# Performance work log

Measured on AMD Instinct MI355X. Metric: run time of the kernel, lower is better.

## Reference

```python
import jax, jax.numpy as jnp
import numpy as np

B, S, HID = 1, 2048, 2048
N_HEADS = 16
HEAD_DIM = HID // N_HEADS  # 128
ROPE_THETA = 10000.0
NEG_INF = -1e9


def setup_inputs() -> dict:
    key = jax.random.key(0)
    ks = jax.random.split(key, 5)
    hidden_states = jax.random.normal(ks[0], (B, S, HID), dtype=jnp.float32)
    scale = 1.0 / np.sqrt(HID)
    Wq = jax.random.normal(ks[1], (HID, HID), dtype=jnp.float32) * scale
    Wk = jax.random.normal(ks[2], (HID, HID), dtype=jnp.float32) * scale
    Wv = jax.random.normal(ks[3], (HID, HID), dtype=jnp.float32) * scale
    Wo = jax.random.normal(ks[4], (HID, HID), dtype=jnp.float32) * scale
    # additive causal mask [B, 1, S, S]: 0 on/below diag, -1e9 above
    causal = jnp.tril(jnp.ones((S, S), dtype=bool))
    attention_mask = jnp.where(causal, 0.0, NEG_INF).astype(jnp.float32)[None, None]
    attention_mask = jnp.broadcast_to(attention_mask, (B, 1, S, S))
    position_ids = jnp.broadcast_to(jnp.arange(S, dtype=jnp.int64)[None, :], (B, S))
    return {"hidden_states": hidden_states, "Wq": Wq, "Wk": Wk, "Wv": Wv,
            "Wo": Wo, "attention_mask": attention_mask, "position_ids": position_ids}


def _rotate_half(x):
    x1, x2 = jnp.split(x, 2, axis=-1)
    return jnp.concatenate((-x2, x1), axis=-1)


def _rope_cos_sin(position_ids, head_dim, dtype):
    inv_freq = 1.0 / (ROPE_THETA ** (jnp.arange(0, head_dim, 2, dtype=jnp.float32) / head_dim))
    freqs = position_ids.astype(jnp.float32)[:, :, None] * inv_freq[None, None, :]  # [b, s, d/2]
    emb = jnp.concatenate((freqs, freqs), axis=-1)  # [b, s, d]
    # unsqueeze_dim=1 -> broadcast over heads
    return jnp.cos(emb).astype(dtype)[:, None], jnp.sin(emb).astype(dtype)[:, None]


def reference(hidden_states, Wq, Wk, Wv, Wo, attention_mask, position_ids):
    b, s, h = hidden_states.shape
    d = HEAD_DIM
    def proj(W):
        return (hidden_states @ W.T).reshape(b, s, N_HEADS, d).transpose(0, 2, 1, 3)  # [b,h,s,d]
    q, k, v = proj(Wq), proj(Wk), proj(Wv)
    cos, sin = _rope_cos_sin(position_ids, d, q.dtype)
    q = q * cos + _rotate_half(q) * sin
    k = k * cos + _rotate_half(k) * sin
    scores = jnp.einsum('bhqd,bhkd->bhqk', q, k) / jnp.sqrt(jnp.float32(d))
    scores = scores + attention_mask
    probs = jax.nn.softmax(scores.astype(jnp.float32), axis=-1).astype(q.dtype)
    attn = jnp.einsum('bhqk,bhkd->bhqd', probs, v)
    out = attn.transpose(0, 2, 1, 3).reshape(b, s, h)
    return out @ Wo.T
```

## Files before the change

kernel.cpp:

```cpp
#include <hip/hip_runtime.h>

typedef _Float16 half8 __attribute__((ext_vector_type(8)));
typedef _Float16 half4 __attribute__((ext_vector_type(4)));
typedef float floatx4 __attribute__((ext_vector_type(4)));
typedef float floatx16 __attribute__((ext_vector_type(16)));

#define GLDS(gp, lp) __builtin_amdgcn_global_load_lds( \
    (const __attribute__((address_space(1))) void*)(gp), \
    (__attribute__((address_space(3))) void*)(lp), 16, 0, 0)

__global__ void cvt_f2h5(const float* __restrict__ s0, const float* __restrict__ s1,
                         const float* __restrict__ s2, const float* __restrict__ s3,
                         const float* __restrict__ s4,
                         _Float16* __restrict__ d0, _Float16* __restrict__ d1,
                         _Float16* __restrict__ d2, _Float16* __restrict__ d3,
                         _Float16* __restrict__ d4, int n8) {
  int i = blockIdx.x * 256 + threadIdx.x;
  if (i >= n8) return;
  const float* s; _Float16* d;
  switch (blockIdx.y) {
    case 0: s = s0; d = d0; break;
    case 1: s = s1; d = d1; break;
    case 2: s = s2; d = d2; break;
    case 3: s = s3; d = d3; break;
    default: s = s4; d = d4; break;
  }
  const float4* s4p = (const float4*)s;
  float4 a = s4p[2 * i], b = s4p[2 * i + 1];
  half8 h;
  h[0] = (_Float16)a.x; h[1] = (_Float16)a.y; h[2] = (_Float16)a.z; h[3] = (_Float16)a.w;
  h[4] = (_Float16)b.x; h[5] = (_Float16)b.y; h[6] = (_Float16)b.z; h[7] = (_Float16)b.w;
  *(half8*)(d + 8 * (size_t)i) = h;
}

__global__ __launch_bounds__(256) void transpose_k(const _Float16* __restrict__ src,
                                                   _Float16* __restrict__ dst) {
  __shared__ _Float16 t[64][72];
  const int r0 = blockIdx.y * 64, c0 = blockIdx.x * 64;
  const int tr = threadIdx.x >> 3, tc = (threadIdx.x & 7) * 8;
  #pragma unroll
  for (int p = 0; p < 2; ++p) {
    half8 v = *(const half8*)(src + (size_t)(r0 + p * 32 + tr) * 2048 + c0 + tc);
    *(half8*)&t[p * 32 + tr][tc] = v;
  }
  __syncthreads();
  #pragma unroll
  for (int p = 0; p < 2; ++p) {
    half8 v;
    #pragma unroll
    for (int j = 0; j < 8; ++j) v[j] = t[tc + j][p * 32 + tr];
    *(half8*)(dst + (size_t)(c0 + p * 32 + tr) * 2048 + r0 + tc) = v;
  }
}

__global__ __launch_bounds__(512, 1) void gemm_qkv(const _Float16* __restrict__ A,
                                                   const _Float16* __restrict__ W,
                                                   _Float16* __restrict__ Cq) {
  extern __shared__ _Float16 lds[];
  _Float16* As = lds;
  _Float16* Bs = lds + 3 * 16384;

  const int tid = threadIdx.x, lane = tid & 63, wv = tid >> 6;
  const int fr = lane & 15, fg = lane >> 4;
  const int wm = wv >> 2, wn = wv & 3;
  const int bm = blockIdx.y * 256, bn = blockIdx.x * 192;
  const _Float16* Ab = A + (size_t)bm * 2048;
  const _Float16* Bb = W + (size_t)bn * 2048;

  const int srow = lane >> 3;
  const int sgr = (lane & 7) ^ srow;

  auto stageA = [&](int t) {
    _Float16* dst = As + (t % 3) * 16384;
    const size_t coff = (size_t)t * 64 + sgr * 8;
    #pragma unroll
    for (int i = 0; i < 4; ++i) {
      const int rb = wv * 32 + i * 8;
      GLDS(Ab + (size_t)(rb + srow) * 2048 + coff, dst + rb * 64);
    }
  };
  auto stageB = [&](int t) {
    _Float16* dst = Bs + (t & 1) * 12288;
    const size_t coff = (size_t)t * 64 + sgr * 8;
    #pragma unroll
    for (int i = 0; i < 3; ++i) {
      const int rb = wv * 24 + i * 8;
      GLDS(Bb + (size_t)(rb + srow) * 2048 + coff, dst + rb * 64);
    }
  };

  const int arow = wm * 128 + fr;
  const int brow = wn * 48 + fr;
  const int sw = fr & 7;

  floatx4 acc[8][3] = {};

  stageA(0); stageB(0); stageA(1);
  asm volatile("s_waitcnt vmcnt(4)" ::: "memory");
  __builtin_amdgcn_s_barrier();

  for (int t = 0; t < 32; ++t) {
    const _Float16* Ac = As + (t % 3) * 16384;
    const _Float16* Bc = Bs + (t & 1) * 12288;
    #pragma unroll
    for (int p = 0; p < 4; ++p) {
      const int kh = p >> 1, qm = p & 1;
      const int sl = ((kh * 4 + fg) ^ sw) * 8;
      half8 af[4], bf[3];
      #pragma unroll
      for (int m = 0; m < 4; ++m)
        af[m] = *(const half8*)(Ac + (arow + qm * 64 + m * 16) * 64 + sl);
      #pragma unroll
      for (int n = 0; n < 3; ++n)
        bf[n] = *(const half8*)(Bc + (brow + n * 16) * 64 + sl);
      if (p == 0 && t + 1 < 32) stageB(t + 1);
      if (p == 2 && t + 2 < 32) stageA(t + 2);
      __builtin_amdgcn_s_barrier();
      asm volatile("s_waitcnt lgkmcnt(0)" ::: "memory");
      __builtin_amdgcn_sched_barrier(0);
      __builtin_amdgcn_s_setprio(1);
      #pragma unroll
      for (int m = 0; m < 4; ++m)
        #pragma unroll
        for (int n = 0; n < 3; ++n)
          acc[qm * 4 + m][n] =
              __builtin_amdgcn_mfma_f32_16x16x32_f16(af[m], bf[n], acc[qm * 4 + m][n], 0, 0, 0);
      __builtin_amdgcn_s_setprio(0);
      if (p == 3) {
        if (t < 30)       asm volatile("s_waitcnt vmcnt(4)" ::: "memory");
        else if (t == 30) asm volatile("s_waitcnt vmcnt(0)" ::: "memory");
      }
      __builtin_amdgcn_s_barrier();
    }
  }

  #pragma unroll
  for (int m = 0; m < 8; ++m)
    #pragma unroll
    for (int n = 0; n < 3; ++n)
      #pragma unroll
      for (int i = 0; i < 4; ++i) {
        const int row = bm + wm * 128 + m * 16 + fg * 4 + i;
        const int col = bn + wn * 48 + n * 16 + fr;
        Cq[(size_t)(col >> 11) * 4194304 + (size_t)row * 2048 + (col & 2047)] =
            (_Float16)acc[m][n][i];
      }
}

template <int OUTF, int BN>
__global__ __launch_bounds__(256) void gemm_nt(const _Float16* __restrict__ A,
                                               const _Float16* __restrict__ B,
                                               _Float16* __restrict__ Ch,
                                               float* __restrict__ Cf,
                                               long long bStride, long long cStride) {
  __shared__ _Float16 As[2][128 * 32];
  __shared__ _Float16 Bs[2][BN * 32];
  const int NF = BN / 32;
  const int tid = threadIdx.x, lane = tid & 63, wv = tid >> 6;
  const int fr = lane & 15, fg = lane >> 4;
  const int bm = blockIdx.y * 128, bn = blockIdx.x * BN;
  const _Float16* Ab = A + (size_t)bm * 2048;
  const _Float16* Bb = B + (size_t)blockIdx.z * bStride + (size_t)bn * 2048;
  const int srow = lane >> 2;
  const int gsw = (lane & 3) ^ ((lane >> 3) & 3);
  const int asw = (fr >> 1) & 3;

  floatx4 acc[4][NF] = {};

  auto stage = [&](int buf, int kt) {
    #pragma unroll
    for (int r = 0; r < 2; ++r) {
      int row = r * 64 + wv * 16 + srow;
      GLDS(Ab + (size_t)row * 2048 + kt * 32 + gsw * 8, &As[buf][(r * 64 + wv * 16) * 32]);
    }
    #pragma unroll
    for (int r = 0; r < BN / 64; ++r) {
      int row = r * 64 + wv * 16 + srow;
      GLDS(Bb + (size_t)row * 2048 + kt * 32 + gsw * 8, &Bs[buf][(r * 64 + wv * 16) * 32]);
    }
  };
  const int wm = (wv >> 1) * 64, wn = (wv & 1) * (BN / 2);

  stage(0, 0);
  __syncthreads();

  #pragma unroll 2
  for (int kt = 0; kt < 64; ++kt) {
    const int cur = kt & 1;
    if (kt < 63) stage(cur ^ 1, kt + 1);
    half8 af[4], bf[NF];
    #pragma unroll
    for (int m = 0; m < 4; ++m)
      af[m] = *(const half8*)&As[cur][(wm + m * 16 + fr) * 32 + ((fg ^ asw) * 8)];
    #pragma unroll
    for (int n = 0; n < NF; ++n)
      bf[n] = *(const half8*)&Bs[cur][(wn + n * 16 + fr) * 32 + ((fg ^ asw) * 8)];
    #pragma unroll
    for (int m = 0; m < 4; ++m)
      #pragma unroll
      for (int n = 0; n < NF; ++n)
        acc[m][n] = __builtin_amdgcn_mfma_f32_16x16x32_f16(af[m], bf[n], acc[m][n], 0, 0, 0);
    __syncthreads();
  }

  #pragma unroll
  for (int m = 0; m < 4; ++m)
    #pragma unroll
    for (int n = 0; n < NF; ++n)
      #pragma unroll
      for (int i = 0; i < 4; ++i) {
        const int row = bm + wm + m * 16 + fg * 4 + i;
        const int col = bn + wn + n * 16 + fr;
        if (OUTF)
          Cf[(size_t)row * 2048 + col] = acc[m][n][i];
        else
          Ch[(size_t)blockIdx.z * cStride + (size_t)row * 2048 + col] = (_Float16)acc[m][n][i];
      }
}

__global__ void rope_k(_Float16* __restrict__ Q, _Float16* __restrict__ K) {
  const int idx = blockIdx.x * 256 + threadIdx.x;
  const int s = idx >> 10;
  const int hd = idx & 1023;
  const int head = hd >> 6, d = hd & 63;
  const float freq = exp2f((float)d * -0.2076205059304601f);
  const float ang = (float)s * freq;
  float sn, c;
  __sincosf(ang, &sn, &c);
  const size_t base = (size_t)s * 2048 + head * 128 + d;
  float q1 = (float)Q[base], q2 = (float)Q[base + 64];
  Q[base]      = (_Float16)(q1 * c - q2 * sn);
  Q[base + 64] = (_Float16)(q2 * c + q1 * sn);
  float k1 = (float)K[base], k2 = (float)K[base + 64];
  K[base]      = (_Float16)(k1 * c - k2 * sn);
  K[base + 64] = (_Float16)(k2 * c + k1 * sn);
}

__global__ __launch_bounds__(256, 2) void attn_k(const _Float16* __restrict__ Qp,
                                                 const _Float16* __restrict__ Kp,
                                                 const _Float16* __restrict__ Vt,
                                                 _Float16* __restrict__ Po,
                                                 float* __restrict__ Pr) {
  extern __shared__ _Float16 smem[];
  _Float16* Ks = smem;
  _Float16* Vs = smem + 2 * 64 * 128;
  _Float16* Pb = smem + 4 * 64 * 128;

  const int tid = threadIdx.x, lane = tid & 63, wv = tid >> 6;
  const int l31 = lane & 31, hi = lane >> 5;
  const int wq = wv >> 1, wk = wv & 1;

  const int bid = (int)blockIdx.x;
  const int head = ((bid & 7) << 1) | ((bid >> 3) & 1);
  const int L = bid >> 4;
  int g, it0, itEnd;
  if (L < 16) { g = 16 + L; it0 = 0; itEnd = 16; }
  else {
    const int j = (L - 16) >> 1;
    if ((L & 1) == 0) { g = 15 - j; it0 = 0; itEnd = g + 1; }
    else             { g = 31 - j; it0 = 16; itEnd = g + 1; }
  }
  const size_t hoff = (size_t)head * 128;
  const int qw = g * 64 + wq * 32;
  _Float16* Pw = Pb + wv * (32 * 40);

  half8 qf[8];
  const _Float16 scl = (_Float16)0.08838834764831845f;
  #pragma unroll
  for (int ks = 0; ks < 8; ++ks) {
    half8 t = *(const half8*)(Qp + (size_t)(qw + l31) * 2048 + hoff + ks * 16 + hi * 8);
    #pragma unroll
    for (int j = 0; j < 8; ++j) t[j] = (_Float16)(t[j] * scl);
    qf[ks] = t;
  }

  auto stage = [&](int buf, int it) {
    const int kv0 = it * 64;
    #pragma unroll
    for (int i = 0; i < 4; ++i) {
      const int rbase = wv * 16 + i * 4;
      const int row = rbase + (lane >> 4);
      const int gr = (lane & 15) ^ (row & 7);
      GLDS(Kp + (size_t)(kv0 + row) * 2048 + hoff + gr * 8,
           Ks + buf * 8192 + rbase * 128);
    }
    #pragma unroll
    for (int i = 0; i < 4; ++i) {
      const int rbase = wv * 32 + i * 8;
      const int row = rbase + (lane >> 3);
      const int gr = (lane & 7) ^ (row & 7);
      GLDS(Vt + (size_t)(hoff + row) * 2048 + kv0 + gr * 8,
           Vs + buf * 8192 + rbase * 64);
    }
  };

  floatx16 o[4] = {};
  float rsum = 0.0f;

  stage(0, it0);
  __syncthreads();

  int buf = 0;
  for (int it = it0; it < itEnd; ++it) {
    if (it + 1 < itEnd) stage(buf ^ 1, it + 1);
    const _Float16* Kb = Ks + buf * 8192;
    const _Float16* Vb = Vs + buf * 8192;

    const int krow = wk * 32 + l31;
    const int ksw = l31 & 7;
    floatx16 S = {};
    __builtin_amdgcn_s_setprio(1);
    #pragma unroll
    for (int ks = 0; ks < 8; ++ks) {
      half8 a = *(const half8*)(Kb + krow * 128 + (((ks * 2 + hi) ^ ksw) * 8));
      S = __builtin_amdgcn_mfma_f32_32x32x16_f16(a, qf[ks], S, 0, 0, 0);
    }
    __builtin_amdgcn_s_setprio(0);

    if (it == g) {
      const int kv0 = it * 64;
      const int qa = qw + l31;
      #pragma unroll
      for (int r = 0; r < 16; ++r) {
        const int ka = kv0 + wk * 32 + (r & 3) + 8 * (r >> 2) + 4 * hi;
        if (ka > qa) S[r] = -1e30f;
      }
    }

    #pragma unroll
    for (int r4 = 0; r4 < 4; ++r4) {
      float p0 = __expf(S[4 * r4 + 0] - 8.0f);
      float p1 = __expf(S[4 * r4 + 1] - 8.0f);
      float p2 = __expf(S[4 * r4 + 2] - 8.0f);
      float p3 = __expf(S[4 * r4 + 3] - 8.0f);
      rsum += (p0 + p1) + (p2 + p3);
      half4 pk;
      pk[0] = (_Float16)p0; pk[1] = (_Float16)p1;
      pk[2] = (_Float16)p2; pk[3] = (_Float16)p3;
      *(half4*)(Pw + l31 * 40 + r4 * 8 + hi * 4) = pk;
    }

    half8 pa0 = *(const half8*)(Pw + l31 * 40 + hi * 8);
    half8 pa1 = *(const half8*)(Pw + l31 * 40 + 16 + hi * 8);

    __builtin_amdgcn_s_setprio(1);
    #pragma unroll
    for (int dt = 0; dt < 4; ++dt) {
      const int vrow = dt * 32 + l31;
      const int vsw = vrow & 7;
      half8 b0 = *(const half8*)(Vb + vrow * 64 + (((wk * 4 + hi) ^ vsw) * 8));
      half8 b1 = *(const half8*)(Vb + vrow * 64 + (((wk * 4 + 2 + hi) ^ vsw) * 8));
      o[dt] = __builtin_amdgcn_mfma_f32_32x32x16_f16(pa0, b0, o[dt], 0, 0, 0);
      o[dt] = __builtin_amdgcn_mfma_f32_32x32x16_f16(pa1, b1, o[dt], 0, 0, 0);
    }
    __builtin_amdgcn_s_setprio(0);

    __syncthreads();
    buf ^= 1;
  }

  float* Mo = (float*)smem;
  float* Mr = (float*)(smem + 16384);
  if (wk == 1) {
    #pragma unroll
    for (int dt = 0; dt < 4; ++dt)
      #pragma unroll
      for (int r = 0; r < 16; ++r)
        Mo[((wq * 4 + dt) * 16 + r) * 64 + lane] = o[dt][r];
    Mr[wq * 64 + lane] = rsum;
  }
  __syncthreads();
  if (wk == 0) {
    rsum += Mr[wq * 64 + lane];
    float rs = rsum;
    rs += __shfl_xor(rs, 32);
    if (hi == 0) Pr[(size_t)bid * 64 + wq * 32 + l31] = rs;
    #pragma unroll
    for (int dt = 0; dt < 4; ++dt)
      #pragma unroll
      for (int r = 0; r < 16; ++r) {
        const float w = o[dt][r] + Mo[((wq * 4 + dt) * 16 + r) * 64 + lane];
        const int ql = wq * 32 + (r & 3) + 8 * (r >> 2) + 4 * hi;
        Po[(size_t)bid * 8192 + ql * 128 + dt * 32 + l31] = (_Float16)w;
      }
  }
}

__global__ __launch_bounds__(256) void attn_merge(const _Float16* __restrict__ Po,
                                                  const float* __restrict__ Pr,
                                                  _Float16* __restrict__ At) {
  const int bidx = (int)blockIdx.x;
  const int h = bidx & 15, g = bidx >> 4;
  const int hb = ((h & 1) << 3) | (h >> 1);
  const int L0 = (g >= 16) ? (g - 16) : (16 + 2 * (15 - g));
  const int U0 = L0 * 16 + hb;
  const bool two = (g >= 16);
  const int U1 = two ? ((17 + 2 * (31 - g)) * 16 + hb) : 0;
  const int t = threadIdx.x;
  const int q = t >> 2, cs = t & 3;
  const float r0 = Pr[(size_t)U0 * 64 + q];
  const float r1 = two ? Pr[(size_t)U1 * 64 + q] : 0.0f;
  const float inv = 1.0f / (r0 + r1);
  const size_t orow = (size_t)(g * 64 + q) * 2048 + h * 128;
  #pragma unroll
  for (int s = 0; s < 4; ++s) {
    const int d0 = (cs + s * 4) * 8;
    half8 a = *(const half8*)(Po + (size_t)U0 * 8192 + q * 128 + d0);
    half8 o;
    if (two) {
      half8 b = *(const half8*)(Po + (size_t)U1 * 8192 + q * 128 + d0);
      #pragma unroll
      for (int j = 0; j < 8; ++j) o[j] = (_Float16)(((float)a[j] + (float)b[j]) * inv);
    } else {
      #pragma unroll
      for (int j = 0; j < 8; ++j) o[j] = (_Float16)((float)a[j] * inv);
    }
    *(half8*)(At + orow + d0) = o;
  }
}

extern "C" void kernel_launch(void* const* d_in, const int* in_sizes, int n_in,
                              void* d_out, int out_size, void* d_ws, size_t ws_size,
                              hipStream_t stream) {
  (void)in_sizes; (void)n_in; (void)out_size; (void)ws_size;
  const float* X  = (const float*)d_in[0];
  const float* Wq = (const float*)d_in[1];
  const float* Wk = (const float*)d_in[2];
  const float* Wv = (const float*)d_in[3];
  const float* Wo = (const float*)d_in[4];
  float* out = (float*)d_out;

  const size_t SZ = 2048ull * 2048ull;
  _Float16* ws  = (_Float16*)d_ws;
  _Float16* Xh  = ws + 0 * SZ;
  _Float16* Wqh = ws + 1 * SZ;
  _Float16* Wkh = ws + 2 * SZ;
  _Float16* Wvh = ws + 3 * SZ;
  _Float16* Woh = ws + 4 * SZ;
  _Float16* Qp  = ws + 5 * SZ;
  _Float16* Kp  = ws + 6 * SZ;
  _Float16* Vp  = ws + 7 * SZ;
  _Float16* Vtg = Wqh;
  _Float16* At  = Xh;
  _Float16* Po  = Wkh;
  float*    Pr  = (float*)Vp;

  const int n8 = (int)(SZ / 8);
  dim3 blk(256);

  cvt_f2h5<<<dim3(n8 / 256, 5), blk, 0, stream>>>(X, Wq, Wk, Wv, Wo,
                                                  Xh, Wqh, Wkh, Wvh, Woh, n8);

  gemm_qkv<<<dim3(32, 8), dim3(512), 147456, stream>>>(Xh, Wqh, Qp);
  rope_k<<<(2048 * 1024) / 256, blk, 0, stream>>>(Qp, Kp);
  transpose_k<<<dim3(32, 32), blk, 0, stream>>>(Vp, Vtg);

  const size_t attn_lds = (4 * 64 * 128 + 4 * 32 * 40) * sizeof(_Float16);
  attn_k<<<768, blk, attn_lds, stream>>>(Qp, Kp, Vtg, Po, Pr);
  attn_merge<<<512, blk, 0, stream>>>(Po, Pr, At);

  gemm_nt<1, 128><<<dim3(16, 16, 1), blk, 0, stream>>>(At, Woh, nullptr, out, 0, 0);
}
```

Before: 168.7 us.

## Fuse split-KV attention merge into output projection GEMM A-tile loading

```diff
diff --git a/kernel.cpp b/kernel.cpp
--- a/kernel.cpp
+++ b/kernel.cpp
@@ -144,77 +144,6 @@
         const int col = bn + wn * 48 + n * 16 + fr;
         Cq[(size_t)(col >> 11) * 4194304 + (size_t)row * 2048 + (col & 2047)] =
             (_Float16)acc[m][n][i];
-      }
-}
-
-template <int OUTF, int BN>
-__global__ __launch_bounds__(256) void gemm_nt(const _Float16* __restrict__ A,
-                                               const _Float16* __restrict__ B,
-                                               _Float16* __restrict__ Ch,
-                                               float* __restrict__ Cf,
-                                               long long bStride, long long cStride) {
-  __shared__ _Float16 As[2][128 * 32];
-  __shared__ _Float16 Bs[2][BN * 32];
-  const int NF = BN / 32;
-  const int tid = threadIdx.x, lane = tid & 63, wv = tid >> 6;
-  const int fr = lane & 15, fg = lane >> 4;
-  const int bm = blockIdx.y * 128, bn = blockIdx.x * BN;
-  const _Float16* Ab = A + (size_t)bm * 2048;
-  const _Float16* Bb = B + (size_t)blockIdx.z * bStride + (size_t)bn * 2048;
-  const int srow = lane >> 2;
-  const int gsw = (lane & 3) ^ ((lane >> 3) & 3);
-  const int asw = (fr >> 1) & 3;
-
-  floatx4 acc[4][NF] = {};
-
-  auto stage = [&](int buf, int kt) {
-    #pragma unroll
-    for (int r = 0; r < 2; ++r) {
-      int row = r * 64 + wv * 16 + srow;
-      GLDS(Ab + (size_t)row * 2048 + kt * 32 + gsw * 8, &As[buf][(r * 64 + wv * 16) * 32]);
-    }
-    #pragma unroll
-    for (int r = 0; r < BN / 64; ++r) {
-      int row = r * 64 + wv * 16 + srow;
-      GLDS(Bb + (size_t)row * 2048 + kt * 32 + gsw * 8, &Bs[buf][(r * 64 + wv * 16) * 32]);
-    }
-  };
-  const int wm = (wv >> 1) * 64, wn = (wv & 1) * (BN / 2);
-
-  stage(0, 0);
-  __syncthreads();
-
-  #pragma unroll 2
-  for (int kt = 0; kt < 64; ++kt) {
-    const int cur = kt & 1;
-    if (kt < 63) stage(cur ^ 1, kt + 1);
-    half8 af[4], bf[NF];
-    #pragma unroll
-    for (int m = 0; m < 4; ++m)
-      af[m] = *(const half8*)&As[cur][(wm + m * 16 + fr) * 32 + ((fg ^ asw) * 8)];
-    #pragma unroll
-    for (int n = 0; n < NF; ++n)
-      bf[n] = *(const half8*)&Bs[cur][(wn + n * 16 + fr) * 32 + ((fg ^ asw) * 8)];
-    #pragma unroll
-    for (int m = 0; m < 4; ++m)
-      #pragma unroll
-      for (int n = 0; n < NF; ++n)
-        acc[m][n] = __builtin_amdgcn_mfma_f32_16x16x32_f16(af[m], bf[n], acc[m][n], 0, 0, 0);
-    __syncthreads();
-  }
-
-  #pragma unroll
-  for (int m = 0; m < 4; ++m)
-    #pragma unroll
-    for (int n = 0; n < NF; ++n)
-      #pragma unroll
-      for (int i = 0; i < 4; ++i) {
-        const int row = bm + wm + m * 16 + fg * 4 + i;
-        const int col = bn + wn + n * 16 + fr;
-        if (OUTF)
-          Cf[(size_t)row * 2048 + col] = acc[m][n][i];
-        else
-          Ch[(size_t)blockIdx.z * cStride + (size_t)row * 2048 + col] = (_Float16)acc[m][n][i];
       }
 }
 
@@ -386,37 +315,108 @@
   }
 }
 
-__global__ __launch_bounds__(256) void attn_merge(const _Float16* __restrict__ Po,
-                                                  const float* __restrict__ Pr,
-                                                  _Float16* __restrict__ At) {
-  const int bidx = (int)blockIdx.x;
-  const int h = bidx & 15, g = bidx >> 4;
-  const int hb = ((h & 1) << 3) | (h >> 1);
-  const int L0 = (g >= 16) ? (g - 16) : (16 + 2 * (15 - g));
-  const int U0 = L0 * 16 + hb;
-  const bool two = (g >= 16);
-  const int U1 = two ? ((17 + 2 * (31 - g)) * 16 + hb) : 0;
-  const int t = threadIdx.x;
-  const int q = t >> 2, cs = t & 3;
-  const float r0 = Pr[(size_t)U0 * 64 + q];
-  const float r1 = two ? Pr[(size_t)U1 * 64 + q] : 0.0f;
-  const float inv = 1.0f / (r0 + r1);
-  const size_t orow = (size_t)(g * 64 + q) * 2048 + h * 128;
-  #pragma unroll
-  for (int s = 0; s < 4; ++s) {
-    const int d0 = (cs + s * 4) * 8;
-    half8 a = *(const half8*)(Po + (size_t)U0 * 8192 + q * 128 + d0);
+__global__ __launch_bounds__(256) void gemm_out(const _Float16* __restrict__ Po,
+                                                const float* __restrict__ Pr,
+                                                const _Float16* __restrict__ Wo,
+                                                float* __restrict__ out) {
+  __shared__ _Float16 As[2][128 * 32];
+  __shared__ _Float16 Bs[2][128 * 32];
+  const int tid = threadIdx.x, lane = tid & 63, wv = tid >> 6;
+  const int fr = lane & 15, fg = lane >> 4;
+  const int bm = blockIdx.y * 128, bn = blockIdx.x * 128;
+  const _Float16* Bb = Wo + (size_t)bn * 2048;
+  const int srow = lane >> 2;
+  const int gsw = (lane & 3) ^ ((lane >> 3) & 3);
+  const int asw = (fr >> 1) & 3;
+  const int wm = (wv >> 1) * 64, wn = (wv & 1) * 64;
+  const int cg = tid & 3;
+  const int r0 = tid >> 2;
+
+  auto stageB = [&](int buf, int kt) {
+    #pragma unroll
+    for (int r = 0; r < 2; ++r) {
+      int row = r * 64 + wv * 16 + srow;
+      GLDS(Bb + (size_t)row * 2048 + kt * 32 + gsw * 8, &Bs[buf][(r * 64 + wv * 16) * 32]);
+    }
+  };
+
+  auto loadA = [&](int kt, int pr, half8& a, half8& b, float& iv, bool& tw) {
+    const int h = kt >> 2, dbase = (kt & 3) * 32;
+    const int hb = ((h & 1) << 3) | (h >> 1);
+    const int r = r0 + pr * 64;
+    const int q = bm + r;
+    const int g = q >> 6, ql = q & 63;
+    tw = (g >= 16);
+    const int L0 = tw ? (g - 16) : (16 + 2 * (15 - g));
+    const int U0 = L0 * 16 + hb;
+    a = *(const half8*)(Po + (size_t)U0 * 8192 + ql * 128 + dbase + cg * 8);
+    float rs = Pr[(size_t)U0 * 64 + ql];
+    if (tw) {
+      const int U1 = (17 + 2 * (31 - g)) * 16 + hb;
+      b = *(const half8*)(Po + (size_t)U1 * 8192 + ql * 128 + dbase + cg * 8);
+      rs += Pr[(size_t)U1 * 64 + ql];
+    }
+    iv = 1.0f / rs;
+  };
+  auto writeA = [&](int buf, int pr, half8 a, half8 b, float iv, bool tw) {
+    const int r = r0 + pr * 64;
     half8 o;
-    if (two) {
-      half8 b = *(const half8*)(Po + (size_t)U1 * 8192 + q * 128 + d0);
-      #pragma unroll
-      for (int j = 0; j < 8; ++j) o[j] = (_Float16)(((float)a[j] + (float)b[j]) * inv);
-    } else {
-      #pragma unroll
-      for (int j = 0; j < 8; ++j) o[j] = (_Float16)((float)a[j] * inv);
-    }
-    *(half8*)(At + orow + d0) = o;
-  }
+    #pragma unroll
+    for (int j = 0; j < 8; ++j) {
+      const float v = (float)a[j] + (tw ? (float)b[j] : 0.0f);
+      o[j] = (_Float16)(v * iv);
+    }
+    *(half8*)&As[buf][r * 32 + ((cg ^ ((r >> 1) & 3)) * 8)] = o;
+  };
+
+  floatx4 acc[4][4] = {};
+  half8 pa[2] = {}, pb[2] = {};
+  float iv[2];
+  bool tw[2];
+
+  stageB(0, 0);
+  #pragma unroll
+  for (int pr = 0; pr < 2; ++pr) loadA(0, pr, pa[pr], pb[pr], iv[pr], tw[pr]);
+  #pragma unroll
+  for (int pr = 0; pr < 2; ++pr) writeA(0, pr, pa[pr], pb[pr], iv[pr], tw[pr]);
+  __syncthreads();
+
+  for (int kt = 0; kt < 64; ++kt) {
+    const int cur = kt & 1;
+    if (kt < 63) {
+      stageB(cur ^ 1, kt + 1);
+      #pragma unroll
+      for (int pr = 0; pr < 2; ++pr) loadA(kt + 1, pr, pa[pr], pb[pr], iv[pr], tw[pr]);
+    }
+    half8 af[4], bf[4];
+    #pragma unroll
+    for (int m = 0; m < 4; ++m)
+      af[m] = *(const half8*)&As[cur][(wm + m * 16 + fr) * 32 + ((fg ^ asw) * 8)];
+    #pragma unroll
+    for (int n = 0; n < 4; ++n)
+      bf[n] = *(const half8*)&Bs[cur][(wn + n * 16 + fr) * 32 + ((fg ^ asw) * 8)];
+    #pragma unroll
+    for (int m = 0; m < 4; ++m)
+      #pragma unroll
+      for (int n = 0; n < 4; ++n)
+        acc[m][n] = __builtin_amdgcn_mfma_f32_16x16x32_f16(af[m], bf[n], acc[m][n], 0, 0, 0);
+    if (kt < 63) {
+      #pragma unroll
+      for (int pr = 0; pr < 2; ++pr) writeA(cur ^ 1, pr, pa[pr], pb[pr], iv[pr], tw[pr]);
+    }
+    __syncthreads();
+  }
+
+  #pragma unroll
+  for (int m = 0; m < 4; ++m)
+    #pragma unroll
+    for (int n = 0; n < 4; ++n)
+      #pragma unroll
+      for (int i = 0; i < 4; ++i) {
+        const int row = bm + wm + m * 16 + fg * 4 + i;
+        const int col = bn + wn + n * 16 + fr;
+        out[(size_t)row * 2048 + col] = acc[m][n][i];
+      }
 }
 
 extern "C" void kernel_launch(void* const* d_in, const int* in_sizes, int n_in,
@@ -441,7 +441,6 @@
   _Float16* Kp  = ws + 6 * SZ;
   _Float16* Vp  = ws + 7 * SZ;
   _Float16* Vtg = Wqh;
-  _Float16* At  = Xh;
   _Float16* Po  = Wkh;
   float*    Pr  = (float*)Vp;
 
@@ -457,7 +456,6 @@
 
   const size_t attn_lds = (4 * 64 * 128 + 4 * 32 * 40) * sizeof(_Float16);
   attn_k<<<768, blk, attn_lds, stream>>>(Qp, Kp, Vtg, Po, Pr);
-  attn_merge<<<512, blk, 0, stream>>>(Po, Pr, At);
-
-  gemm_nt<1, 128><<<dim3(16, 16, 1), blk, 0, stream>>>(At, Woh, nullptr, out, 0, 0);
-}
+
+  gemm_out<<<dim3(16, 16), blk, 0, stream>>>(Po, Pr, Woh, out);
+}
```

Result: slower. 191.5 us (median of 2 runs) (+13.6%).
